# Kernel tuning notes

Measured on AMD Instinct MI355X. Metric: run time of the kernel, lower is better.

Reference implementation:

```python
import jax, jax.numpy as jnp
import numpy as np

EMBED_DIM = 768
N_HEADS = 12
TIME_RATIO = 0.5
HEAD_DIM = EMBED_DIM // N_HEADS          # 64
T_HEAD = int(HEAD_DIM * TIME_RATIO)      # 32 time dims per head
T_DIM = T_HEAD * N_HEADS                 # 384 time dims overall
EPS = 1e-5


def _ln(v, g, b):
    m = jnp.mean(v, axis=-1, keepdims=True)
    var = jnp.mean((v - m) ** 2, axis=-1, keepdims=True)
    return (v - m) * jax.lax.rsqrt(var + EPS) * g + b


def minkowski_ln(x, g_t, b_t, g_s, b_s):
    # normalize time-like and space-like channel groups separately
    xt, xs = x[..., :T_DIM], x[..., T_DIM:]
    return jnp.concatenate([_ln(xt, g_t, b_t), _ln(xs, g_s, b_s)], axis=-1)


def lorentz_attention(x, Wq, bq, Wk, bk, Wv, bv, Wo, bo):
    B, S, D = x.shape
    def heads(W, b):
        return (x @ W + b).reshape(B, S, N_HEADS, HEAD_DIM).transpose(0, 2, 1, 3)
    q, k, v = heads(Wq, bq), heads(Wk, bk), heads(Wv, bv)
    # Minkowski metric signature (-,...,-,+,...,+) within each head
    eta = jnp.concatenate([-jnp.ones((T_HEAD,), x.dtype), jnp.ones((HEAD_DIM - T_HEAD,), x.dtype)])
    logits = jnp.einsum('bhqd,bhkd->bhqk', q * eta, k) / np.sqrt(HEAD_DIM).astype(np.float32)
    attn = jax.nn.softmax(logits, axis=-1)
    o = jnp.einsum('bhqk,bhkd->bhqd', attn, v)
    o = o.transpose(0, 2, 1, 3).reshape(B, S, D)
    return o @ Wo + bo


def setup_inputs() -> dict:
    key = jax.random.key(0)
    ks = jax.random.split(key, 16)
    D, H4 = EMBED_DIM, EMBED_DIM * 4
    s = 0.02
    inp = {
        'x': jax.random.normal(ks[0], (2, 2048, D), jnp.float32),
        'Wq': jax.random.normal(ks[1], (D, D), jnp.float32) * s, 'bq': jnp.zeros((D,), jnp.float32),
        'Wk': jax.random.normal(ks[2], (D, D), jnp.float32) * s, 'bk': jnp.zeros((D,), jnp.float32),
        'Wv': jax.random.normal(ks[3], (D, D), jnp.float32) * s, 'bv': jnp.zeros((D,), jnp.float32),
        'Wo': jax.random.normal(ks[4], (D, D), jnp.float32) * s, 'bo': jnp.zeros((D,), jnp.float32),
        'g1t': jnp.ones((T_DIM,), jnp.float32), 'b1t': jnp.zeros((T_DIM,), jnp.float32),
        'g1s': jnp.ones((D - T_DIM,), jnp.float32), 'b1s': jnp.zeros((D - T_DIM,), jnp.float32),
        'W1': jax.random.normal(ks[5], (D, H4), jnp.float32) * s, 'bb1': jnp.zeros((H4,), jnp.float32),
        'W2': jax.random.normal(ks[6], (H4, D), jnp.float32) * s, 'bb2': jnp.zeros((D,), jnp.float32),
        'g2t': jnp.ones((T_DIM,), jnp.float32), 'b2t': jnp.zeros((T_DIM,), jnp.float32),
        'g2s': jnp.ones((D - T_DIM,), jnp.float32), 'b2s': jnp.zeros((D - T_DIM,), jnp.float32),
    }
    return inp


def reference(x, Wq, bq, Wk, bk, Wv, bv, Wo, bo,
              g1t, b1t, g1s, b1s, W1, bb1, W2, bb2,
              g2t, b2t, g2s, b2s):
    a = lorentz_attention(x, Wq, bq, Wk, bk, Wv, bv, Wo, bo)
    x = minkowski_ln(x + a, g1t, b1t, g1s, b1s)
    h = jax.nn.gelu(x @ W1 + bb1) @ W2 + bb2
    x = minkowski_ln(x + h, g2t, b2t, g2s, b2s)
    return x
```

## Files before the change

### kernel.cpp

```cpp
#include <hip/hip_runtime.h>
#include <cstddef>
#include <cstdint>

#define D_EMB  768
#define NHEAD  12
#define HDIM   64
#define THEAD  32
#define SEQ    2048
#define BATCH  2
#define NROW   (BATCH*SEQ)
#define HID4   3072

typedef unsigned short u16;
typedef __bf16 bf16x8 __attribute__((ext_vector_type(8)));
typedef float  f32x4  __attribute__((ext_vector_type(4)));
typedef unsigned short u16x8 __attribute__((ext_vector_type(8)));

__device__ __forceinline__ u16 f2bf(float f) {
    unsigned u = __builtin_bit_cast(unsigned, f);
    return (u16)((u + 0x7FFFu + ((u >> 16) & 1u)) >> 16);
}
__device__ __forceinline__ float bf2f(u16 h) {
    return __builtin_bit_cast(float, (unsigned)h << 16);
}
__device__ __forceinline__ u16 cvt_bf(float f) {
    return __builtin_bit_cast(u16, (__bf16)f);
}

__device__ __forceinline__ void gload_lds16(const void* g, void* l) {
    __builtin_amdgcn_global_load_lds(
        reinterpret_cast<const __attribute__((address_space(1))) void*>(
            reinterpret_cast<uintptr_t>(g)),
        reinterpret_cast<__attribute__((address_space(3))) void*>(
            (uint32_t)reinterpret_cast<uintptr_t>(l)),
        16, 0, 0);
}

__device__ __forceinline__ void tcast(float (*t)[33], const float* __restrict__ W,
                                      u16* __restrict__ WT, int K, int M,
                                      int mt, int kt)
{
    const int m0 = mt * 32, k0 = kt * 32;
    const int tx = threadIdx.x & 31, ty = threadIdx.x >> 5;
#pragma unroll
    for (int i = 0; i < 32; i += 8)
        t[ty + i][tx] = W[(size_t)(k0 + ty + i) * M + m0 + tx];
    __syncthreads();
#pragma unroll
    for (int i = 0; i < 32; i += 8)
        WT[(size_t)(m0 + ty + i) * K + k0 + tx] = f2bf(t[tx][ty + i]);
}

__global__ __launch_bounds__(256)
void prep(const float* __restrict__ Wq, const float* __restrict__ Wk,
          const float* __restrict__ Wv, const float* __restrict__ Wo,
          const float* __restrict__ W1, const float* __restrict__ W2,
          const float* __restrict__ bq, const float* __restrict__ bk,
          const float* __restrict__ bv, const float* __restrict__ x,
          u16* __restrict__ WqkvoT, u16* __restrict__ W1T,
          u16* __restrict__ W2T, u16* __restrict__ xb,
          float* __restrict__ bqkv)
{
    __shared__ float t[32][33];
    const int bid = blockIdx.x;
    if (bid < 2304) {
        const int z = bid / 576, r = bid % 576;
        const float* W = z == 0 ? Wq : z == 1 ? Wk : z == 2 ? Wv : Wo;
        tcast(t, W, WqkvoT + (size_t)z * 768 * 768, 768, 768, r % 24, r / 24);
    } else if (bid < 4608) {
        const int r = bid - 2304;
        tcast(t, W1, W1T, 768, 3072, r % 96, r / 96);
    } else if (bid < 6912) {
        const int r = bid - 4608;
        tcast(t, W2, W2T, 3072, 768, r % 24, r / 24);
    } else if (bid < 8448) {
        const int i = (bid - 6912) * 2048 + threadIdx.x * 8;
        const float4 a = *reinterpret_cast<const float4*>(x + i);
        const float4 b = *reinterpret_cast<const float4*>(x + i + 4);
        u16x8 h;
        h[0] = f2bf(a.x); h[1] = f2bf(a.y); h[2] = f2bf(a.z); h[3] = f2bf(a.w);
        h[4] = f2bf(b.x); h[5] = f2bf(b.y); h[6] = f2bf(b.z); h[7] = f2bf(b.w);
        *reinterpret_cast<u16x8*>(xb + i) = h;
    } else {
        const int i = (bid - 8448) * 256 + threadIdx.x;
        if (i < 2304)
            bqkv[i] = i < 768 ? bq[i] : (i < 1536 ? bk[i - 768] : bv[i - 1536]);
    }
}

template<int EPI>
__global__ __launch_bounds__(256)
void gemm_bf16(const u16* __restrict__ A, const u16* __restrict__ B,
               const float* __restrict__ bias, void* __restrict__ Cp,
               u16* __restrict__ VTp, int K, int N)
{
    __shared__ u16 As[2][128 * 32];
    __shared__ u16 Bs[2][128 * 32];
    const int tid  = threadIdx.x;
    const int lane = tid & 63;
    const int w    = tid >> 6;
    const int m0 = blockIdx.x * 128, n0 = blockIdx.y * 128;
    const int wr = (w >> 1) << 6, wc = (w & 1) << 6;

    const int seg0 = (w << 11) + lane * 16;
    const int row0 = seg0 >> 6, cb0 = (seg0 & 63) >> 1;
    const int seg1 = seg0 + 1024;
    const int row1 = seg1 >> 6, cb1 = (seg1 & 63) >> 1;
    const u16* a0 = A + (size_t)(m0 + row0) * K + cb0;
    const u16* a1 = A + (size_t)(m0 + row1) * K + cb1;
    const u16* b0 = B + (size_t)(n0 + row0) * K + cb0;
    const u16* b1 = B + (size_t)(n0 + row1) * K + cb1;
    const int lo0 = (w * 2 + 0) << 9;
    const int lo1 = (w * 2 + 1) << 9;

    int aIdx[4], bIdx[4];
#pragma unroll
    for (int i = 0; i < 4; ++i) {
        aIdx[i] = (wr + i * 16 + (lane & 15)) * 32 + ((lane >> 4) << 3);
        bIdx[i] = (wc + i * 16 + (lane & 15)) * 32 + ((lane >> 4) << 3);
    }

    f32x4 acc[4][4];
#pragma unroll
    for (int i = 0; i < 4; ++i)
#pragma unroll
        for (int j = 0; j < 4; ++j)
#pragma unroll
            for (int q = 0; q < 4; ++q) acc[i][j][q] = 0.f;

    gload_lds16(a0, &As[0][lo0]);
    gload_lds16(a1, &As[0][lo1]);
    gload_lds16(b0, &Bs[0][lo0]);
    gload_lds16(b1, &Bs[0][lo1]);
    __syncthreads();

    int cur = 0;
    for (int k0 = 0; k0 < K; k0 += 32) {
        if (k0 + 32 < K) {
            gload_lds16(a0 + k0 + 32, &As[cur ^ 1][lo0]);
            gload_lds16(a1 + k0 + 32, &As[cur ^ 1][lo1]);
            gload_lds16(b0 + k0 + 32, &Bs[cur ^ 1][lo0]);
            gload_lds16(b1 + k0 + 32, &Bs[cur ^ 1][lo1]);
        }
        bf16x8 af[4], bv[4];
#pragma unroll
        for (int i = 0; i < 4; ++i)
            af[i] = *reinterpret_cast<const bf16x8*>(&As[cur][aIdx[i]]);
#pragma unroll
        for (int j = 0; j < 4; ++j)
            bv[j] = *reinterpret_cast<const bf16x8*>(&Bs[cur][bIdx[j]]);
#pragma unroll
        for (int i = 0; i < 4; ++i)
#pragma unroll
            for (int j = 0; j < 4; ++j)
                acc[i][j] = __builtin_amdgcn_mfma_f32_16x16x32_bf16(
                    af[i], bv[j], acc[i][j], 0, 0, 0);
        __syncthreads();
        cur ^= 1;
    }

#pragma unroll
    for (int i = 0; i < 4; ++i) {
#pragma unroll
        for (int q = 0; q < 4; ++q) {
            const int row = m0 + wr + i * 16 + ((lane >> 4) << 2) + q;
#pragma unroll
            for (int j = 0; j < 4; ++j) {
                const int col = n0 + wc + j * 16 + (lane & 15);
                float v = acc[i][j][q] + bias[col];
                if (EPI == 2) {
                    const float z = 1.5957691216057308f *
                                    (v + 0.044715f * v * v * v);
                    const float e = __builtin_amdgcn_exp2f(z * -1.4426950408889634f);
                    v = v * __builtin_amdgcn_rcpf(1.f + e);
                    ((u16*)Cp)[(size_t)row * N + col] = cvt_bf(v);
                } else {
                    if (n0 < 1536) {
                        ((u16*)Cp)[(size_t)row * 1536 + col] = cvt_bf(v);
                    } else {
                        const int c2 = col - 1536;
                        const int hh = c2 >> 6, dd = c2 & 63;
                        const int bb = row >> 11, tok = row & 2047;
                        const int t = tok & 63;
                        const int p = ((t & 15) << 2) | (t >> 4);
                        VTp[((size_t)(bb * NHEAD + hh) * HDIM + dd) * SEQ
                            + (tok & ~63) + p] = cvt_bf(v);
                    }
                }
            }
        }
    }
}

__global__ __launch_bounds__(256)
void gemm_n64(const u16* __restrict__ A, const u16* __restrict__ B,
              const float* __restrict__ bias, float* __restrict__ C0,
              float* __restrict__ C1, int Khalf, int Ktot, int N)
{
    __shared__ u16 As[2][64 * 32];
    __shared__ u16 Bs[2][128 * 32];
    const int tid  = threadIdx.x;
    const int lane = tid & 63;
    const int w    = tid >> 6;
    const int l15  = lane & 15;
    const int g    = lane >> 4;
    const int m0 = blockIdx.x * 64, n0 = blockIdx.y * 128;
    const int zz = blockIdx.z;
    const int kbase = zz * Khalf;
    float* __restrict__ C = zz ? C1 : C0;

    const int segA = (w << 10) + lane * 16;
    const int rowA = segA >> 6, cbA = (segA & 63) >> 1;
    const u16* aP = A + (size_t)(m0 + rowA) * Ktot + kbase + cbA;
    const int loA = w << 9;
    const int seg0 = (w << 11) + lane * 16;
    const int row0 = seg0 >> 6, cb0 = (seg0 & 63) >> 1;
    const int seg1 = seg0 + 1024;
    const int row1 = seg1 >> 6, cb1 = (seg1 & 63) >> 1;
    const u16* b0 = B + (size_t)(n0 + row0) * Ktot + kbase + cb0;
    const u16* b1 = B + (size_t)(n0 + row1) * Ktot + kbase + cb1;
    const int lo0 = w << 10, lo1 = (w << 10) + 512;

    int aIdx[4], bIdx[2];
#pragma unroll
    for (int i = 0; i < 4; ++i) aIdx[i] = (i * 16 + l15) * 32 + (g << 3);
#pragma unroll
    for (int j = 0; j < 2; ++j) bIdx[j] = ((w << 5) + j * 16 + l15) * 32 + (g << 3);

    f32x4 acc[4][2];
#pragma unroll
    for (int i = 0; i < 4; ++i)
#pragma unroll
        for (int j = 0; j < 2; ++j)
#pragma unroll
            for (int q = 0; q < 4; ++q) acc[i][j][q] = 0.f;

    gload_lds16(aP, &As[0][loA]);
    gload_lds16(b0, &Bs[0][lo0]);
    gload_lds16(b1, &Bs[0][lo1]);
    __syncthreads();

    int cur = 0;
    for (int k0 = 0; k0 < Khalf; k0 += 32) {
        if (k0 + 32 < Khalf) {
            gload_lds16(aP + k0 + 32, &As[cur ^ 1][loA]);
            gload_lds16(b0 + k0 + 32, &Bs[cur ^ 1][lo0]);
            gload_lds16(b1 + k0 + 32, &Bs[cur ^ 1][lo1]);
        }
        bf16x8 af[4], bv[2];
#pragma unroll
        for (int i = 0; i < 4; ++i)
            af[i] = *reinterpret_cast<const bf16x8*>(&As[cur][aIdx[i]]);
#pragma unroll
        for (int j = 0; j < 2; ++j)
            bv[j] = *reinterpret_cast<const bf16x8*>(&Bs[cur][bIdx[j]]);
#pragma unroll
        for (int i = 0; i < 4; ++i)
#pragma unroll
            for (int j = 0; j < 2; ++j)
                acc[i][j] = __builtin_amdgcn_mfma_f32_16x16x32_bf16(
                    af[i], bv[j], acc[i][j], 0, 0, 0);
        __syncthreads();
        cur ^= 1;
    }

#pragma unroll
    for (int i = 0; i < 4; ++i) {
#pragma unroll
        for (int q = 0; q < 4; ++q) {
            const int row = m0 + i * 16 + (g << 2) + q;
#pragma unroll
            for (int j = 0; j < 2; ++j) {
                const int col = n0 + (w << 5) + j * 16 + l15;
                const float bb = zz ? 0.f : bias[col];
                C[(size_t)row * N + col] = acc[i][j][q] + bb;
            }
        }
    }
}

#define SM_SCALE 0.18033688011112042f

__global__ __launch_bounds__(256)
void attn_mfma(const u16* __restrict__ QK, const u16* __restrict__ VT,
               u16* __restrict__ O)
{
    __shared__ u16 Ks[2][64 * 64];
    __shared__ u16 Vs[2][64 * 64];
    __shared__ u16 Ps[64 * 72];

    const int tid  = threadIdx.x;
    const int lane = tid & 63;
    const int w    = tid >> 6;
    const int l15  = lane & 15;
    const int g    = lane >> 4;
    const int bh   = blockIdx.x;
    const int b    = bh / NHEAD, h = bh % NHEAD;
    const int q0   = blockIdx.y * 64;
    const int bS   = b * SEQ;

    bf16x8 aq[2];
    {
        const u16* Qg = QK + (size_t)(bS + q0 + (w << 4) + l15) * 1536 + h * HDIM;
#pragma unroll
        for (int kk = 0; kk < 2; ++kk) {
            const u16x8 hq = *reinterpret_cast<const u16x8*>(Qg + kk * 32 + g * 8);
            const float sc = (kk == 0) ? -SM_SCALE : SM_SCALE;
            u16x8 hs;
#pragma unroll
            for (int j = 0; j < 8; ++j)
                hs[j] = cvt_bf(bf2f(hq[j]) * sc);
            aq[kk] = __builtin_bit_cast(bf16x8, hs);
        }
    }

    const int rl = lane >> 3;
    const int cs = ((lane & 7) ^ rl) << 3;
    const u16* pK = QK + (size_t)(bS + 16 * w + rl) * 1536 + 768 + h * HDIM + cs;
    const u16* pV = VT + ((size_t)(b * NHEAD + h) * HDIM + 16 * w + rl) * SEQ + cs;

    int swz[2];
#pragma unroll
    for (int kk = 0; kk < 2; ++kk)
        swz[kk] = ((kk * 4 + g) ^ (l15 & 7)) << 3;

    bf16x8 vones;
    {
        u16x8 o16;
#pragma unroll
        for (int j = 0; j < 8; ++j) o16[j] = 0x3F80u;
        vones = __builtin_bit_cast(bf16x8, o16);
    }

    f32x4 accO[4];
#pragma unroll
    for (int n = 0; n < 4; ++n)
#pragma unroll
        for (int q = 0; q < 4; ++q) accO[n][q] = 0.f;
    f32x4 accS;
#pragma unroll
    for (int q = 0; q < 4; ++q) accS[q] = 0.f;

#define ATTN_STAGE(c, kt)                                                   \
    do {                                                                    \
        u16* dK = &Ks[c][w * 1024];                                         \
        u16* dV = &Vs[c][w * 1024];                                         \
        gload_lds16(pK + (size_t)(kt) * 1536,       dK);                    \
        gload_lds16(pK + (size_t)((kt) + 8) * 1536, dK + 512);              \
        gload_lds16(pV + (kt),           dV);                               \
        gload_lds16(pV + (kt) + 8 * SEQ, dV + 512);                         \
    } while (0)

    ATTN_STAGE(0, 0);
    __syncthreads();
    int cur = 0;

    for (int kt = 0; kt < SEQ; kt += 64) {
        if (kt + 64 < SEQ) ATTN_STAGE(cur ^ 1, kt + 64);

        f32x4 sac[4];
        __builtin_amdgcn_s_setprio(1);
#pragma unroll
        for (int n = 0; n < 4; ++n) {
#pragma unroll
            for (int q = 0; q < 4; ++q) sac[n][q] = 0.f;
#pragma unroll
            for (int kk = 0; kk < 2; ++kk) {
                const bf16x8 bk = *reinterpret_cast<const bf16x8*>(
                    &Ks[cur][(n * 16 + l15) * 64 + swz[kk]]);
                sac[n] = __builtin_amdgcn_mfma_f32_16x16x32_bf16(
                    aq[kk], bk, sac[n], 0, 0, 0);
            }
        }
        __builtin_amdgcn_s_setprio(0);

#pragma unroll
        for (int r4 = 0; r4 < 4; ++r4) {
            const int prow = (w << 4) + (g << 2) + r4;
            const float sv0 = __builtin_amdgcn_exp2f(sac[0][r4]);
            const float sv1 = __builtin_amdgcn_exp2f(sac[1][r4]);
            const float sv2 = __builtin_amdgcn_exp2f(sac[2][r4]);
            const float sv3 = __builtin_amdgcn_exp2f(sac[3][r4]);
            ushort4 pk4;
            pk4.x = cvt_bf(sv0);
            pk4.y = cvt_bf(sv1);
            pk4.z = cvt_bf(sv2);
            pk4.w = cvt_bf(sv3);
            *reinterpret_cast<ushort4*>(&Ps[prow * 72 + (l15 << 2)]) = pk4;
        }

        bf16x8 pa[2];
#pragma unroll
        for (int kk = 0; kk < 2; ++kk)
            pa[kk] = *reinterpret_cast<const bf16x8*>(
                &Ps[((w << 4) + l15) * 72 + kk * 32 + g * 8]);
        __builtin_amdgcn_s_setprio(1);
#pragma unroll
        for (int n = 0; n < 4; ++n) {
#pragma unroll
            for (int kk = 0; kk < 2; ++kk) {
                const bf16x8 bv = *reinterpret_cast<const bf16x8*>(
                    &Vs[cur][(n * 16 + l15) * 64 + swz[kk]]);
                accO[n] = __builtin_amdgcn_mfma_f32_16x16x32_bf16(
                    pa[kk], bv, accO[n], 0, 0, 0);
            }
        }
#pragma unroll
        for (int kk = 0; kk < 2; ++kk)
            accS = __builtin_amdgcn_mfma_f32_16x16x32_bf16(
                pa[kk], vones, accS, 0, 0, 0);
        __builtin_amdgcn_s_setprio(0);
        __syncthreads();
        cur ^= 1;
    }

#pragma unroll
    for (int r4 = 0; r4 < 4; ++r4) {
        const float inv = 1.f / accS[r4];
        const int qr = q0 + (w << 4) + (g << 2) + r4;
#pragma unroll
        for (int n = 0; n < 4; ++n)
            O[(size_t)(bS + qr) * D_EMB + h * HDIM + n * 16 + l15]
                = cvt_bf(accO[n][r4] * inv);
    }
#undef ATTN_STAGE
}

template<int XBF, int WF32>
__global__ __launch_bounds__(256)
void mink_ln(const void* __restrict__ Xp, const float* __restrict__ R1,
             const float* __restrict__ R2,
             const float* __restrict__ gt, const float* __restrict__ bt,
             const float* __restrict__ gs, const float* __restrict__ bs,
             float* __restrict__ Out, u16* __restrict__ OutB, int nrows)
{
    const int wid  = (int)((blockIdx.x * 256 + threadIdx.x) >> 6);
    const int lane = threadIdx.x & 63;
    const int row  = wid >> 1, half = wid & 1;
    if (row >= nrows) return;

    const float* g  = half ? gs : gt;
    const float* bb = half ? bs : bt;
    const size_t base = (size_t)row * D_EMB + half * 384;

    float v[6];
    float sum = 0.f;
#pragma unroll
    for (int i = 0; i < 6; ++i) {
        const size_t e = base + i * 64 + lane;
        const float xv = XBF ? bf2f(((const u16*)Xp)[e]) : ((const float*)Xp)[e];
        const float t = xv + R1[e] + R2[e];
        v[i] = t; sum += t;
    }
#pragma unroll
    for (int off = 32; off; off >>= 1) sum += __shfl_xor(sum, off);
    const float mean = sum * (1.f / 384.f);

    float ss = 0.f;
#pragma unroll
    for (int i = 0; i < 6; ++i) { const float d = v[i] - mean; ss += d * d; }
#pragma unroll
    for (int off = 32; off; off >>= 1) ss += __shfl_xor(ss, off);
    const float rstd = rsqrtf(ss * (1.f / 384.f) + 1e-5f);

#pragma unroll
    for (int i = 0; i < 6; ++i) {
        const int e = i * 64 + lane;
        const float o = (v[i] - mean) * rstd * g[e] + bb[e];
        if (WF32) Out[base + e] = o;
        if (OutB) OutB[base + e] = cvt_bf(o);
    }
}

extern "C" void kernel_launch(void* const* d_in, const int* in_sizes, int n_in,
                              void* d_out, int out_size, void* d_ws, size_t ws_size,
                              hipStream_t stream)
{
    const float* x   = (const float*)d_in[0];
    const float* Wq  = (const float*)d_in[1];
    const float* bq  = (const float*)d_in[2];
    const float* Wk  = (const float*)d_in[3];
    const float* bk  = (const float*)d_in[4];
    const float* Wv  = (const float*)d_in[5];
    const float* bv  = (const float*)d_in[6];
    const float* Wo  = (const float*)d_in[7];
    const float* bo  = (const float*)d_in[8];
    const float* g1t = (const float*)d_in[9];
    const float* b1t = (const float*)d_in[10];
    const float* g1s = (const float*)d_in[11];
    const float* b1s = (const float*)d_in[12];
    const float* W1  = (const float*)d_in[13];
    const float* bb1 = (const float*)d_in[14];
    const float* W2  = (const float*)d_in[15];
    const float* bb2 = (const float*)d_in[16];
    const float* g2t = (const float*)d_in[17];
    const float* b2t = (const float*)d_in[18];
    const float* g2s = (const float*)d_in[19];
    const float* b2s = (const float*)d_in[20];
    float* out = (float*)d_out;

    const size_t ND = (size_t)NROW * D_EMB;
    u16* WqkvoT = (u16*)d_ws;
    u16* W1T = WqkvoT + 2359296;
    u16* W2T = W1T + 2359296;
    u16* xb  = W2T + 2359296;
    u16* QKb = xb + ND;
    u16* VTb = QKb + (size_t)NROW * 1536;
    u16* Ab  = VTb + ND;
    u16* Hb  = QKb;
    float* QKf  = (float*)QKb;
    float* AoF  = (float*)(Ab + ND);
    float* bqkv = AoF;

    const dim3 blk(256);

    prep<<<8457, blk, 0, stream>>>(Wq, Wk, Wv, Wo, W1, W2, bq, bk, bv, x,
                                   WqkvoT, W1T, W2T, xb, bqkv);

    gemm_bf16<3><<<dim3(32, 18), blk, 0, stream>>>(xb, WqkvoT, bqkv, QKb, VTb,
                                                   768, 2304);
    attn_mfma<<<dim3(BATCH * NHEAD, SEQ / 64), blk, 0, stream>>>(QKb, VTb, Ab);

    gemm_n64<<<dim3(64, 6, 2), blk, 0, stream>>>(
        Ab, WqkvoT + (size_t)2304 * 768, bo, AoF, QKf, 384, 768, 768);
    mink_ln<0, 0><<<2048, blk, 0, stream>>>(x, AoF, QKf, g1t, b1t, g1s, b1s,
                                            nullptr, xb, NROW);
    gemm_bf16<2><<<dim3(32, 24), blk, 0, stream>>>(xb, W1T, bb1, Hb, nullptr,
                                                   768, 3072);
    gemm_n64<<<dim3(64, 6, 2), blk, 0, stream>>>(
        Hb, W2T, bb2, AoF, out, 1536, 3072, 768);
    mink_ln<1, 1><<<2048, blk, 0, stream>>>(xb, AoF, out, g2t, b2t, g2s, b2s,
                                            out, nullptr, NROW);
}
```

Baseline: 179.8 us.

## Switch attention to 32x32 MFMA tiles with split-K over keys and merge

Attention now uses 32x32x16 MFMA with 128-query blocks per workgroup. The key range is split into two halves along a new grid dimension, each producing unnormalized partial outputs and row sums, which a new merge kernel adds and normalizes. The row sum now comes from register accumulation instead of an extra MFMA against a ones vector, and V is stored untransposed within each tile. This gives more work per tile and keeps a similar block count, at the cost of an extra launch and extra memory traffic for the bf16 partials, plus some precision loss from rounding the partials to bf16.

```diff
diff --git a/kernel.cpp b/kernel.cpp
--- a/kernel.cpp
+++ b/kernel.cpp
@@ -14,6 +14,7 @@
 typedef unsigned short u16;
 typedef __bf16 bf16x8 __attribute__((ext_vector_type(8)));
 typedef float  f32x4  __attribute__((ext_vector_type(4)));
+typedef float  f32x16 __attribute__((ext_vector_type(16)));
 typedef unsigned short u16x8 __attribute__((ext_vector_type(8)));
 
 __device__ __forceinline__ u16 f2bf(float f) {
@@ -181,10 +182,8 @@
                         const int c2 = col - 1536;
                         const int hh = c2 >> 6, dd = c2 & 63;
                         const int bb = row >> 11, tok = row & 2047;
-                        const int t = tok & 63;
-                        const int p = ((t & 15) << 2) | (t >> 4);
-                        VTp[((size_t)(bb * NHEAD + hh) * HDIM + dd) * SEQ
-                            + (tok & ~63) + p] = cvt_bf(v);
+                        VTp[((size_t)(bb * NHEAD + hh) * HDIM + dd) * SEQ + tok]
+                            = cvt_bf(v);
                     }
                 }
             }
@@ -283,63 +282,54 @@
 
 __global__ __launch_bounds__(256)
 void attn_mfma(const u16* __restrict__ QK, const u16* __restrict__ VT,
-               u16* __restrict__ O)
+               u16* __restrict__ O0, u16* __restrict__ O1,
+               float* __restrict__ Sp)
 {
     __shared__ u16 Ks[2][64 * 64];
     __shared__ u16 Vs[2][64 * 64];
-    __shared__ u16 Ps[64 * 72];
+    __shared__ u16 Ps[128 * 72];
 
     const int tid  = threadIdx.x;
     const int lane = tid & 63;
     const int w    = tid >> 6;
-    const int l15  = lane & 15;
-    const int g    = lane >> 4;
+    const int l31  = lane & 31;
+    const int hi   = lane >> 5;
     const int bh   = blockIdx.x;
     const int b    = bh / NHEAD, h = bh % NHEAD;
-    const int q0   = blockIdx.y * 64;
+    const int q0   = blockIdx.y * 128;
+    const int z    = blockIdx.z;
+    const int keybase = z * 1024;
     const int bS   = b * SEQ;
 
-    bf16x8 aq[2];
+    bf16x8 bq[4];
     {
-        const u16* Qg = QK + (size_t)(bS + q0 + (w << 4) + l15) * 1536 + h * HDIM;
-#pragma unroll
-        for (int kk = 0; kk < 2; ++kk) {
-            const u16x8 hq = *reinterpret_cast<const u16x8*>(Qg + kk * 32 + g * 8);
-            const float sc = (kk == 0) ? -SM_SCALE : SM_SCALE;
+        const u16* Qg = QK + (size_t)(bS + q0 + w * 32 + l31) * 1536 + h * HDIM;
+#pragma unroll
+        for (int s = 0; s < 4; ++s) {
+            const u16x8 hq = *reinterpret_cast<const u16x8*>(
+                Qg + (s * 2 + hi) * 8);
+            const float sc = (s < 2) ? -SM_SCALE : SM_SCALE;
             u16x8 hs;
 #pragma unroll
             for (int j = 0; j < 8; ++j)
                 hs[j] = cvt_bf(bf2f(hq[j]) * sc);
-            aq[kk] = __builtin_bit_cast(bf16x8, hs);
+            bq[s] = __builtin_bit_cast(bf16x8, hs);
         }
     }
 
     const int rl = lane >> 3;
     const int cs = ((lane & 7) ^ rl) << 3;
-    const u16* pK = QK + (size_t)(bS + 16 * w + rl) * 1536 + 768 + h * HDIM + cs;
-    const u16* pV = VT + ((size_t)(b * NHEAD + h) * HDIM + 16 * w + rl) * SEQ + cs;
-
-    int swz[2];
-#pragma unroll
-    for (int kk = 0; kk < 2; ++kk)
-        swz[kk] = ((kk * 4 + g) ^ (l15 & 7)) << 3;
-
-    bf16x8 vones;
-    {
-        u16x8 o16;
-#pragma unroll
-        for (int j = 0; j < 8; ++j) o16[j] = 0x3F80u;
-        vones = __builtin_bit_cast(bf16x8, o16);
-    }
-
-    f32x4 accO[4];
-#pragma unroll
-    for (int n = 0; n < 4; ++n)
-#pragma unroll
-        for (int q = 0; q < 4; ++q) accO[n][q] = 0.f;
-    f32x4 accS;
-#pragma unroll
-    for (int q = 0; q < 4; ++q) accS[q] = 0.f;
+    const u16* pK = QK + (size_t)(bS + keybase + 16 * w + rl) * 1536
+                    + 768 + h * HDIM + cs;
+    const u16* pV = VT + ((size_t)(b * NHEAD + h) * HDIM + 16 * w + rl) * SEQ
+                    + keybase + cs;
+
+    f32x16 accO[2];
+#pragma unroll
+    for (int dt = 0; dt < 2; ++dt)
+#pragma unroll
+        for (int r = 0; r < 16; ++r) accO[dt][r] = 0.f;
+    float psum = 0.f;
 
 #define ATTN_STAGE(c, kt)                                                   \
     do {                                                                    \
@@ -355,75 +345,101 @@
     __syncthreads();
     int cur = 0;
 
-    for (int kt = 0; kt < SEQ; kt += 64) {
-        if (kt + 64 < SEQ) ATTN_STAGE(cur ^ 1, kt + 64);
-
-        f32x4 sac[4];
+    for (int kt = 0; kt < 1024; kt += 64) {
+        if (kt + 64 < 1024) ATTN_STAGE(cur ^ 1, kt + 64);
+
+        f32x16 sac[2];
         __builtin_amdgcn_s_setprio(1);
 #pragma unroll
-        for (int n = 0; n < 4; ++n) {
-#pragma unroll
-            for (int q = 0; q < 4; ++q) sac[n][q] = 0.f;
-#pragma unroll
-            for (int kk = 0; kk < 2; ++kk) {
-                const bf16x8 bk = *reinterpret_cast<const bf16x8*>(
-                    &Ks[cur][(n * 16 + l15) * 64 + swz[kk]]);
-                sac[n] = __builtin_amdgcn_mfma_f32_16x16x32_bf16(
-                    aq[kk], bk, sac[n], 0, 0, 0);
+        for (int t = 0; t < 2; ++t) {
+#pragma unroll
+            for (int r = 0; r < 16; ++r) sac[t][r] = 0.f;
+#pragma unroll
+            for (int s = 0; s < 4; ++s) {
+                const int key = t * 32 + l31;
+                const int ch  = (s * 2 + hi) ^ (key & 7);
+                const bf16x8 ak = *reinterpret_cast<const bf16x8*>(
+                    &Ks[cur][key * 64 + ch * 8]);
+                sac[t] = __builtin_amdgcn_mfma_f32_32x32x16_bf16(
+                    ak, bq[s], sac[t], 0, 0, 0);
             }
         }
         __builtin_amdgcn_s_setprio(0);
 
-#pragma unroll
-        for (int r4 = 0; r4 < 4; ++r4) {
-            const int prow = (w << 4) + (g << 2) + r4;
-            const float sv0 = __builtin_amdgcn_exp2f(sac[0][r4]);
-            const float sv1 = __builtin_amdgcn_exp2f(sac[1][r4]);
-            const float sv2 = __builtin_amdgcn_exp2f(sac[2][r4]);
-            const float sv3 = __builtin_amdgcn_exp2f(sac[3][r4]);
-            ushort4 pk4;
-            pk4.x = cvt_bf(sv0);
-            pk4.y = cvt_bf(sv1);
-            pk4.z = cvt_bf(sv2);
-            pk4.w = cvt_bf(sv3);
-            *reinterpret_cast<ushort4*>(&Ps[prow * 72 + (l15 << 2)]) = pk4;
-        }
-
-        bf16x8 pa[2];
-#pragma unroll
-        for (int kk = 0; kk < 2; ++kk)
-            pa[kk] = *reinterpret_cast<const bf16x8*>(
-                &Ps[((w << 4) + l15) * 72 + kk * 32 + g * 8]);
+        const int prow = (w * 32 + l31) * 72;
+#pragma unroll
+        for (int t = 0; t < 2; ++t) {
+#pragma unroll
+            for (int grp = 0; grp < 4; ++grp) {
+                const float e0 = __builtin_amdgcn_exp2f(sac[t][grp * 4 + 0]);
+                const float e1 = __builtin_amdgcn_exp2f(sac[t][grp * 4 + 1]);
+                const float e2 = __builtin_amdgcn_exp2f(sac[t][grp * 4 + 2]);
+                const float e3 = __builtin_amdgcn_exp2f(sac[t][grp * 4 + 3]);
+                psum += (e0 + e1) + (e2 + e3);
+                ushort4 pk4;
+                pk4.x = cvt_bf(e0); pk4.y = cvt_bf(e1);
+                pk4.z = cvt_bf(e2); pk4.w = cvt_bf(e3);
+                const int key0 = t * 32 + grp * 8 + hi * 4;
+                *reinterpret_cast<ushort4*>(&Ps[prow + key0]) = pk4;
+            }
+        }
+
         __builtin_amdgcn_s_setprio(1);
 #pragma unroll
-        for (int n = 0; n < 4; ++n) {
-#pragma unroll
-            for (int kk = 0; kk < 2; ++kk) {
+        for (int ks = 0; ks < 4; ++ks) {
+            const bf16x8 ap = *reinterpret_cast<const bf16x8*>(
+                &Ps[prow + (ks * 2 + hi) * 8]);
+#pragma unroll
+            for (int dt = 0; dt < 2; ++dt) {
+                const int d  = dt * 32 + l31;
+                const int ch = (ks * 2 + hi) ^ (d & 7);
                 const bf16x8 bv = *reinterpret_cast<const bf16x8*>(
-                    &Vs[cur][(n * 16 + l15) * 64 + swz[kk]]);
-                accO[n] = __builtin_amdgcn_mfma_f32_16x16x32_bf16(
-                    pa[kk], bv, accO[n], 0, 0, 0);
+                    &Vs[cur][d * 64 + ch * 8]);
+                accO[dt] = __builtin_amdgcn_mfma_f32_32x32x16_bf16(
+                    ap, bv, accO[dt], 0, 0, 0);
             }
         }
-#pragma unroll
-        for (int kk = 0; kk < 2; ++kk)
-            accS = __builtin_amdgcn_mfma_f32_16x16x32_bf16(
-                pa[kk], vones, accS, 0, 0, 0);
         __builtin_amdgcn_s_setprio(0);
         __syncthreads();
         cur ^= 1;
     }
 
-#pragma unroll
-    for (int r4 = 0; r4 < 4; ++r4) {
-        const float inv = 1.f / accS[r4];
-        const int qr = q0 + (w << 4) + (g << 2) + r4;
-#pragma unroll
-        for (int n = 0; n < 4; ++n)
-            O[(size_t)(bS + qr) * D_EMB + h * HDIM + n * 16 + l15]
-                = cvt_bf(accO[n][r4] * inv);
-    }
+    psum += __shfl_xor(psum, 32);
+    u16* __restrict__ Oz = z ? O1 : O0;
+#pragma unroll
+    for (int dt = 0; dt < 2; ++dt)
+#pragma unroll
+        for (int r = 0; r < 16; ++r) {
+            const int qr = q0 + w * 32 + (r & 3) + 8 * (r >> 2) + 4 * hi;
+            Oz[(size_t)(bS + qr) * D_EMB + h * HDIM + dt * 32 + l31]
+                = cvt_bf(accO[dt][r]);
+        }
+    if (lane < 32)
+        Sp[(size_t)z * (BATCH * NHEAD * SEQ) + (b * NHEAD + h) * SEQ
+           + q0 + w * 32 + l31] = psum;
 #undef ATTN_STAGE
+}
+
+__global__ __launch_bounds__(256)
+void attn_merge(const u16* __restrict__ O0, const u16* __restrict__ O1,
+                const float* __restrict__ Sp, u16* __restrict__ Ab)
+{
+    const int gid = blockIdx.x * 256 + threadIdx.x;
+    const size_t e = (size_t)gid * 8;
+    const int row = gid / 96;
+    const int cc  = gid % 96;
+    const int h   = cc >> 3;
+    const int b   = row >> 11, q = row & 2047;
+    const int si  = (b * NHEAD + h) * SEQ + q;
+    const float s = Sp[si] + Sp[(size_t)(BATCH * NHEAD * SEQ) + si];
+    const float inv = __builtin_amdgcn_rcpf(s);
+    const u16x8 a = *reinterpret_cast<const u16x8*>(O0 + e);
+    const u16x8 c = *reinterpret_cast<const u16x8*>(O1 + e);
+    u16x8 o;
+#pragma unroll
+    for (int j = 0; j < 8; ++j)
+        o[j] = cvt_bf((bf2f(a[j]) + bf2f(c[j])) * inv);
+    *reinterpret_cast<u16x8*>(Ab + e) = o;
 }
 
 template<int XBF, int WF32>
@@ -511,6 +527,9 @@
     float* QKf  = (float*)QKb;
     float* AoF  = (float*)(Ab + ND);
     float* bqkv = AoF;
+    u16* Op0 = (u16*)AoF;
+    u16* Op1 = Op0 + ND;
+    float* Sp = (float*)xb;
 
     const dim3 blk(256);
 
@@ -519,7 +538,9 @@
 
     gemm_bf16<3><<<dim3(32, 18), blk, 0, stream>>>(xb, WqkvoT, bqkv, QKb, VTb,
                                                    768, 2304);
-    attn_mfma<<<dim3(BATCH * NHEAD, SEQ / 64), blk, 0, stream>>>(QKb, VTb, Ab);
+    attn_mfma<<<dim3(BATCH * NHEAD, SEQ / 128, 2), blk, 0, stream>>>(
+        QKb, VTb, Op0, Op1, Sp);
+    attn_merge<<<(int)(ND / 8 / 256), blk, 0, stream>>>(Op0, Op1, Sp, Ab);
 
     gemm_n64<<<dim3(64, 6, 2), blk, 0, stream>>>(
         Ab, WqkvoT + (size_t)2304 * 768, bo, AoF, QKf, 384, 768, 768);
```

After: 183.9 us. +2.2%, slower.
